# Kernel tuning notes

Hardware: AMD Instinct MI355X
Metric: run time of the kernel (lower is better)

The kernel has to match this reference:

```python
import jax, jax.numpy as jnp
import numpy as np

D_MODEL = 1024
N_HEADS = 16
HEAD_DIM = D_MODEL // N_HEADS


def setup_inputs() -> dict:
    key = jax.random.key(0)
    k_x, k_wqkv, k_bqkv, k_wo, k_bo = jax.random.split(key, 5)
    lim_qkv = 1.0 / np.sqrt(D_MODEL)
    return {
        "x": jax.random.normal(k_x, (2, 4096, D_MODEL), dtype=jnp.float32),
        "w_qkv": jax.random.uniform(k_wqkv, (D_MODEL, 3 * D_MODEL), minval=-lim_qkv, maxval=lim_qkv, dtype=jnp.float32),
        "b_qkv": jax.random.uniform(k_bqkv, (3 * D_MODEL,), minval=-lim_qkv, maxval=lim_qkv, dtype=jnp.float32),
        "w_out": jax.random.uniform(k_wo, (D_MODEL, D_MODEL), minval=-lim_qkv, maxval=lim_qkv, dtype=jnp.float32),
        "b_out": jax.random.uniform(k_bo, (D_MODEL,), minval=-lim_qkv, maxval=lim_qkv, dtype=jnp.float32),
    }


def reference(x, w_qkv, b_qkv, w_out, b_out):
    b, s, _ = x.shape
    scale = HEAD_DIM ** -0.5
    qkv = x @ w_qkv + b_qkv                              # [b, s, 3*d]
    qkv = qkv.reshape(b, s, 3, N_HEADS, HEAD_DIM)
    qkv = jnp.transpose(qkv, (2, 0, 3, 1, 4))            # [3, b, h, s, hd]
    q, k, v = qkv[0], qkv[1], qkv[2]
    scores = jnp.einsum("bhqd,bhkd->bhqk", q, k) * scale  # [b, h, s, s]
    causal = jnp.triu(jnp.ones((s, s), dtype=bool), k=1)
    scores = jnp.where(causal, -jnp.inf, scores)
    probs = jax.nn.softmax(scores, axis=-1)
    out = jnp.einsum("bhqk,bhkd->bhqd", probs, v)         # [b, h, s, hd]
    out = jnp.transpose(out, (0, 2, 1, 3)).reshape(b, s, D_MODEL)
    return out @ w_out + b_out
```

## Files before the change

### kernel.cpp

```cpp
#include <hip/hip_runtime.h>
#include <math.h>

#define S_LEN 4096
#define DM    1024
#define NHEAD 16
#define HDIM  64
#define C3    3072

typedef __attribute__((ext_vector_type(8))) short bf8_t;
typedef __attribute__((ext_vector_type(4))) float f32x4;
typedef __attribute__((ext_vector_type(16))) float f32x16;

__device__ __forceinline__ short f2bf(float f) {
    union { float f; unsigned u; } v; v.f = f;
    unsigned r = v.u + 0x7FFF + ((v.u >> 16) & 1);
    return (short)(r >> 16);
}
__device__ __forceinline__ float fexp2(float x) { return __builtin_amdgcn_exp2f(x); }

__device__ __forceinline__ unsigned cvtpk(float a, float b) {
    unsigned r;
    asm("v_cvt_pk_bf16_f32 %0, %1, %2" : "=v"(r) : "v"(a), "v"(b));
    return r;
}

__device__ __forceinline__ void gload_lds16(const void* g, void* l) {
    __builtin_amdgcn_global_load_lds(
        (const __attribute__((address_space(1))) unsigned int*)g,
        (__attribute__((address_space(3))) unsigned int*)l, 16, 0, 0);
}

__device__ __forceinline__ float vsum16(f32x16 s) {
    float a = (s[0] + s[1]) + (s[2] + s[3]);
    float b = (s[4] + s[5]) + (s[6] + s[7]);
    float c = (s[8] + s[9]) + (s[10] + s[11]);
    float d = (s[12] + s[13]) + (s[14] + s[15]);
    return (a + b) + (c + d);
}

__global__ void cast_f32_bf16(const float* __restrict__ in, short* __restrict__ out, int n8)
{
    int i = blockIdx.x * blockDim.x + threadIdx.x;
    if (i < n8) {
        float4 a = ((const float4*)in)[i * 2];
        float4 b = ((const float4*)in)[i * 2 + 1];
        bf8_t v = {f2bf(a.x), f2bf(a.y), f2bf(a.z), f2bf(a.w),
                   f2bf(b.x), f2bf(b.y), f2bf(b.z), f2bf(b.w)};
        ((bf8_t*)out)[i] = v;
    }
}

__global__ __launch_bounds__(256)
void transpose_cast(const float* __restrict__ in, short* __restrict__ out, int R, int C)
{
    __shared__ float t[32][33];
    const int tx = threadIdx.x & 31;
    const int ty = threadIdx.x >> 5;
    const int r0 = blockIdx.y * 32;
    const int c0 = blockIdx.x * 32;
    #pragma unroll
    for (int i = 0; i < 32; i += 8)
        t[ty + i][tx] = in[(size_t)(r0 + ty + i) * C + c0 + tx];
    __syncthreads();
    #pragma unroll
    for (int i = 0; i < 32; i += 8)
        out[(size_t)(c0 + ty + i) * R + r0 + tx] = f2bf(t[tx][ty + i]);
}

__global__ __launch_bounds__(256)
void transpose_v(const short* __restrict__ qkv, short* __restrict__ vt)
{
    __shared__ short t[64][72];
    const int st = blockIdx.x, bh = blockIdx.y;
    const int b = bh >> 4, h = bh & 15;
    const int tid = threadIdx.x;
    const int r   = tid >> 2;
    const int c16 = (tid & 3) * 16;
    const short* src = qkv + (size_t)b * S_LEN * C3 + 2 * DM + h * HDIM;
    const short* sp  = src + (size_t)(st * 64 + r) * C3 + c16;
    *(bf8_t*)&t[r][c16]     = *(const bf8_t*)sp;
    *(bf8_t*)&t[r][c16 + 8] = *(const bf8_t*)(sp + 8);
    __syncthreads();
    short tmp[16];
    #pragma unroll
    for (int i = 0; i < 16; ++i) tmp[i] = t[c16 + i][r];
    short* dp = vt + (size_t)bh * HDIM * S_LEN + (size_t)r * S_LEN + st * 64 + c16;
    *(bf8_t*)dp       = *(bf8_t*)&tmp[0];
    *(bf8_t*)(dp + 8) = *(bf8_t*)&tmp[8];
}

template<bool BF16OUT>
__global__ __launch_bounds__(256)
void gemm_mfma(const short* __restrict__ A, const short* __restrict__ Bt,
               const float* __restrict__ bias, void* __restrict__ Cout,
               int M, int N)
{
    constexpr int K = 1024;
    __shared__ __align__(16) short As[128 * 64];
    __shared__ __align__(16) short Bs[128 * 64];

    const int nbx = N / 128;
    const int nwg = (M / 128) * nbx;
    int bid = blockIdx.x;
    bid = (bid & 7) * (nwg >> 3) + (bid >> 3);
    const int by = bid / nbx, bx = bid % nbx;
    const int row0 = by * 128, col0 = bx * 128;

    const int tid  = threadIdx.x;
    const int lane = tid & 63;
    const int w    = tid >> 6;
    const int l15  = lane & 15;
    const int l4   = lane >> 4;
    const int wr   = w >> 1, wc = w & 1;

    f32x4 acc[4][4];
    #pragma unroll
    for (int i = 0; i < 4; ++i)
        #pragma unroll
        for (int j = 0; j < 4; ++j) acc[i][j] = (f32x4){0.f, 0.f, 0.f, 0.f};

    size_t goff[4];
    int    loff[4];
    #pragma unroll
    for (int i = 0; i < 4; ++i) {
        const int o   = (w * 4 + i) * 1024 + lane * 16;
        const int row = o >> 7;
        const int col = (o & 127) ^ ((row & 7) << 4);
        goff[i] = (size_t)row * (K * 2) + col;
        loff[i] = o;
    }
    const char* Ab = (const char*)A  + (size_t)row0 * (K * 2);
    const char* Bb = (const char*)Bt + (size_t)col0 * (K * 2);

    for (int k0 = 0; k0 < K; k0 += 64) {
        __syncthreads();
        #pragma unroll
        for (int i = 0; i < 4; ++i) {
            gload_lds16(Ab + goff[i] + k0 * 2, (char*)As + loff[i]);
            gload_lds16(Bb + goff[i] + k0 * 2, (char*)Bs + loff[i]);
        }
        __syncthreads();

        #pragma unroll
        for (int ks = 0; ks < 2; ++ks) {
            bf8_t af[4], bfr[4];
            #pragma unroll
            for (int mi = 0; mi < 4; ++mi) {
                const int row = wr * 64 + mi * 16 + l15;
                const int off = (row * 128 + ks * 64 + l4 * 16) ^ ((row & 7) << 4);
                af[mi] = *(bf8_t*)((char*)As + off);
            }
            #pragma unroll
            for (int ni = 0; ni < 4; ++ni) {
                const int row = wc * 64 + ni * 16 + l15;
                const int off = (row * 128 + ks * 64 + l4 * 16) ^ ((row & 7) << 4);
                bfr[ni] = *(bf8_t*)((char*)Bs + off);
            }
            #pragma unroll
            for (int mi = 0; mi < 4; ++mi)
                #pragma unroll
                for (int ni = 0; ni < 4; ++ni)
                    acc[mi][ni] = __builtin_amdgcn_mfma_f32_16x16x32_bf16(
                        af[mi], bfr[ni], acc[mi][ni], 0, 0, 0);
        }
    }

    float bv[4];
    #pragma unroll
    for (int ni = 0; ni < 4; ++ni)
        bv[ni] = bias[col0 + wc * 64 + ni * 16 + l15];

    #pragma unroll
    for (int mi = 0; mi < 4; ++mi)
        #pragma unroll
        for (int r = 0; r < 4; ++r) {
            const int row = row0 + wr * 64 + mi * 16 + l4 * 4 + r;
            #pragma unroll
            for (int ni = 0; ni < 4; ++ni) {
                const int col = col0 + wc * 64 + ni * 16 + l15;
                const float val = acc[mi][ni][r] + bv[ni];
                if constexpr (BF16OUT)
                    ((short*)Cout)[(size_t)row * N + col] = f2bf(val);
                else
                    ((float*)Cout)[(size_t)row * N + col] = val;
            }
        }
}

__global__ __launch_bounds__(256)
void attn_mfma32(const short* __restrict__ qkv, const short* __restrict__ vt,
                 short* __restrict__ out)
{
    const int lin = blockIdx.x + 16 * blockIdx.y;
    const int xcd = lin & 7;
    const int idx = lin >> 3;
    const int bh  = xcd * 4 + (idx >> 4);
    const int g   = idx & 15;

    const int b   = bh >> 4, h = bh & 15;
    const int tid = threadIdx.x;
    const int lane = tid & 63;
    const int w    = tid >> 6;
    const int l31  = lane & 31;
    const int hi   = lane >> 5;

    __shared__ __align__(16) short lds[2][2][64 * 64];

    const float C   = 0.125f * 1.44269504f;
    const float NEG = -1e30f;

    const short* qkb = qkv + (size_t)b * S_LEN * C3 + h * HDIM;

    const int sr = tid >> 3;
    const int sc = ((tid & 7) * 16) ^ ((sr & 7) << 4);
    const char* srcK = (const char*)(qkb + DM) + (size_t)sr * (C3 * 2) + sc;
    const char* srcV = (const char*)(vt + (size_t)bh * HDIM * S_LEN)
                       + (size_t)sr * (S_LEN * 2) + sc;
    const int ldst = tid * 16;

    #pragma unroll 1
    for (int half = 0; half < 2; ++half) {
        const int qb     = half ? g : (31 - g);
        const int Q0     = qb * 128;
        const int nkt    = qb * 2 + 2;
        const int qmin_w = Q0 + w * 32;
        const int qmax_w = qmin_w + 31;
        const int q_g    = qmin_w + l31;
        const int nkt_w  = (qmax_w >> 6) + 1;

        bf8_t qf[4];
        {
            const short* qp = qkb + (size_t)q_g * C3 + hi * 8;
            qf[0] = *(const bf8_t*)(qp);
            qf[1] = *(const bf8_t*)(qp + 16);
            qf[2] = *(const bf8_t*)(qp + 32);
            qf[3] = *(const bf8_t*)(qp + 48);
        }

        f32x16 o0, o1;
        #pragma unroll
        for (int r = 0; r < 16; ++r) { o0[r] = 0.f; o1[r] = 0.f; }
        float l = 0.f;

        gload_lds16(srcK,                     (char*)lds + ldst);
        gload_lds16(srcK + 32 * (C3 * 2),     (char*)lds + 4096 + ldst);
        gload_lds16(srcV,                     (char*)lds + 8192 + ldst);
        gload_lds16(srcV + 32 * (S_LEN * 2),  (char*)lds + 12288 + ldst);
        __syncthreads();

        for (int kt = 0; kt < nkt; ++kt) {
            const int cur = kt & 1;
            if (kt + 1 < nkt) {
                const char* sK = srcK + (size_t)(kt + 1) * 64 * (C3 * 2);
                const char* sV = srcV + (size_t)(kt + 1) * 64 * 2;
                char* dstb = (char*)lds + (cur ^ 1) * 16384;
                gload_lds16(sK,                    dstb + ldst);
                gload_lds16(sK + 32 * (C3 * 2),    dstb + 4096 + ldst);
                gload_lds16(sV,                    dstb + 8192 + ldst);
                gload_lds16(sV + 32 * (S_LEN * 2), dstb + 12288 + ldst);
            }

            if (kt < nkt_w) {
                const char* Kb = (char*)lds + cur * 16384;
                const char* Vb = Kb + 8192;
                const int kb0 = kt * 64;
                const bool act1 = (kb0 + 32) <= qmax_w;

                f32x16 s0, s1;
                #pragma unroll
                for (int r = 0; r < 16; ++r) { s0[r] = 0.f; s1[r] = NEG; }
                __builtin_amdgcn_s_setprio(1);
                #pragma unroll
                for (int ds = 0; ds < 4; ++ds) {
                    const int R0 = l31;
                    const int off0 = (R0 * 128 + ds * 32 + hi * 16) ^ ((R0 & 7) << 4);
                    bf8_t kf = *(const bf8_t*)(Kb + off0);
                    s0 = __builtin_amdgcn_mfma_f32_32x32x16_bf16(kf, qf[ds], s0, 0, 0, 0);
                }
                if (act1) {
                    #pragma unroll
                    for (int r = 0; r < 16; ++r) s1[r] = 0.f;
                    #pragma unroll
                    for (int ds = 0; ds < 4; ++ds) {
                        const int R1 = 32 + l31;
                        const int off1 = (R1 * 128 + ds * 32 + hi * 16) ^ ((R1 & 7) << 4);
                        bf8_t kf = *(const bf8_t*)(Kb + off1);
                        s1 = __builtin_amdgcn_mfma_f32_32x32x16_bf16(kf, qf[ds], s1, 0, 0, 0);
                    }
                }
                __builtin_amdgcn_s_setprio(0);

                if (kb0 + 31 > qmin_w) {
                    #pragma unroll
                    for (int r = 0; r < 16; ++r) {
                        const int k = kb0 + 4 * hi + ((r & 3) + 8 * (r >> 2));
                        if (k > q_g) s0[r] = NEG;
                    }
                }
                if (act1 && (kb0 + 63 > qmin_w)) {
                    #pragma unroll
                    for (int r = 0; r < 16; ++r) {
                        const int k = kb0 + 32 + 4 * hi + ((r & 3) + 8 * (r >> 2));
                        if (k > q_g) s1[r] = NEG;
                    }
                }

                #pragma unroll
                for (int r = 0; r < 16; ++r) s0[r] = fexp2(s0[r] * C);
                #pragma unroll
                for (int r = 0; r < 16; ++r) s1[r] = fexp2(s1[r] * C);

                l += vsum16(s0) + vsum16(s1);

                unsigned W0[2][4], W1[2][4];
                #pragma unroll
                for (int gg = 0; gg < 4; ++gg) {
                    W0[0][gg] = cvtpk(s0[4 * gg], s0[4 * gg + 1]);
                    W1[0][gg] = cvtpk(s0[4 * gg + 2], s0[4 * gg + 3]);
                    W0[1][gg] = cvtpk(s1[4 * gg], s1[4 * gg + 1]);
                    W1[1][gg] = cvtpk(s1[4 * gg + 2], s1[4 * gg + 3]);
                }

                #pragma unroll
                for (int c = 0; c < 4; ++c) {
                    const int t  = c >> 1;
                    const int gA = 2 * (c & 1);
                    const int gB = gA + 1;
                    const unsigned rx0 = __shfl_xor(hi ? W0[t][gA] : W0[t][gB], 32);
                    const unsigned rx1 = __shfl_xor(hi ? W1[t][gA] : W1[t][gB], 32);
                    union { unsigned u[4]; bf8_t v; } pf;
                    pf.u[0] = hi ? rx0 : W0[t][gA];
                    pf.u[1] = hi ? rx1 : W1[t][gA];
                    pf.u[2] = hi ? W0[t][gB] : rx0;
                    pf.u[3] = hi ? W1[t][gB] : rx1;

                    __builtin_amdgcn_s_setprio(1);
                    {
                        const int R = l31;
                        const int off = (R * 128 + c * 32 + hi * 16) ^ ((R & 7) << 4);
                        bf8_t vf = *(const bf8_t*)(Vb + off);
                        o0 = __builtin_amdgcn_mfma_f32_32x32x16_bf16(pf.v, vf, o0, 0, 0, 0);
                    }
                    {
                        const int R = 32 + l31;
                        const int off = (R * 128 + c * 32 + hi * 16) ^ ((R & 7) << 4);
                        bf8_t vf = *(const bf8_t*)(Vb + off);
                        o1 = __builtin_amdgcn_mfma_f32_32x32x16_bf16(pf.v, vf, o1, 0, 0, 0);
                    }
                    __builtin_amdgcn_s_setprio(0);
                }
            }
            __syncthreads();
        }

        const float lt = l + __shfl_xor(l, 32);
        const float inv = 1.f / lt;
        #pragma unroll
        for (int r = 0; r < 16; ++r) {
            const int cr = 4 * hi + ((r & 3) + 8 * (r >> 2));
            const float iv = __shfl(inv, cr);
            const int row = Q0 + w * 32 + cr;
            short* op = out + (size_t)(b * S_LEN + row) * DM + h * HDIM + l31;
            op[0]  = f2bf(o0[r] * iv);
            op[32] = f2bf(o1[r] * iv);
        }
    }
}

extern "C" void kernel_launch(void* const* d_in, const int* in_sizes, int n_in,
                              void* d_out, int out_size, void* d_ws, size_t ws_size,
                              hipStream_t stream)
{
    const float* x     = (const float*)d_in[0];
    const float* w_qkv = (const float*)d_in[1];
    const float* b_qkv = (const float*)d_in[2];
    const float* w_out = (const float*)d_in[3];
    const float* b_out = (const float*)d_in[4];
    float* out = (float*)d_out;

    const int M = 2 * S_LEN;

    char* ws = (char*)d_ws;
    short* qkvb  = (short*)(ws);
    short* attnb = (short*)(ws + 50331648);
    short* xb    = (short*)(ws + 67108864);
    short* wqkvT = (short*)(ws + 83886080);
    short* woutT = (short*)(ws + 90177536);
    short* vtb   = (short*)(ws + 92274688);

    cast_f32_bf16<<<dim3((M * DM / 8 + 255) / 256), 256, 0, stream>>>(x, xb, M * DM / 8);
    transpose_cast<<<dim3(C3 / 32, DM / 32), 256, 0, stream>>>(w_qkv, wqkvT, DM, C3);
    transpose_cast<<<dim3(DM / 32, DM / 32), 256, 0, stream>>>(w_out, woutT, DM, DM);

    gemm_mfma<true><<<dim3((M / 128) * (C3 / 128)), 256, 0, stream>>>(
        xb, wqkvT, b_qkv, qkvb, M, C3);

    transpose_v<<<dim3(S_LEN / 64, 2 * NHEAD), 256, 0, stream>>>(qkvb, vtb);

    attn_mfma32<<<dim3(16, 2 * NHEAD), 256, 0, stream>>>(qkvb, vtb, attnb);

    gemm_mfma<false><<<dim3((M / 128) * (DM / 128)), 256, 0, stream>>>(
        attnb, woutT, b_out, out, M, DM);
}
```

Baseline: 224.0 us.

## Software-pipeline attention loop: overlap PV of previous tile with QK softmax

Restructures the attention inner loop so the PV MFMAs for tile kt-1 are issued between the QK MFMAs and the softmax/exp work of tile kt. The aim is to let the matrix units run while the vector units compute exp and pack. To keep the previous tile's V resident, LDS goes from double to triple buffering, and the packed probabilities are carried across iterations in registers. A tail step handles the final tile's PV. The change adds register pressure and LDS use, and it carries a correctness risk in the epilogue condition.

```diff
diff --git a/kernel.cpp b/kernel.cpp
--- a/kernel.cpp
+++ b/kernel.cpp
@@ -204,7 +204,7 @@
     const int l31  = lane & 31;
     const int hi   = lane >> 5;
 
-    __shared__ __align__(16) short lds[2][2][64 * 64];
+    __shared__ __align__(16) char lds[3][16384];
 
     const float C   = 0.125f * 1.44269504f;
     const float NEG = -1e30f;
@@ -241,32 +241,35 @@
         #pragma unroll
         for (int r = 0; r < 16; ++r) { o0[r] = 0.f; o1[r] = 0.f; }
         float l = 0.f;
-
-        gload_lds16(srcK,                     (char*)lds + ldst);
-        gload_lds16(srcK + 32 * (C3 * 2),     (char*)lds + 4096 + ldst);
-        gload_lds16(srcV,                     (char*)lds + 8192 + ldst);
-        gload_lds16(srcV + 32 * (S_LEN * 2),  (char*)lds + 12288 + ldst);
+        unsigned Pf[4][4];
+
+        gload_lds16(srcK,                     lds[0] + ldst);
+        gload_lds16(srcK + 32 * (C3 * 2),     lds[0] + 4096 + ldst);
+        gload_lds16(srcV,                     lds[0] + 8192 + ldst);
+        gload_lds16(srcV + 32 * (S_LEN * 2),  lds[0] + 12288 + ldst);
         __syncthreads();
 
+        int cur = 0;
+        #pragma unroll 1
         for (int kt = 0; kt < nkt; ++kt) {
-            const int cur = kt & 1;
+            const int nxt = (cur == 2) ? 0 : cur + 1;
+            const int prv = (cur == 0) ? 2 : cur - 1;
+
             if (kt + 1 < nkt) {
                 const char* sK = srcK + (size_t)(kt + 1) * 64 * (C3 * 2);
                 const char* sV = srcV + (size_t)(kt + 1) * 64 * 2;
-                char* dstb = (char*)lds + (cur ^ 1) * 16384;
-                gload_lds16(sK,                    dstb + ldst);
-                gload_lds16(sK + 32 * (C3 * 2),    dstb + 4096 + ldst);
-                gload_lds16(sV,                    dstb + 8192 + ldst);
-                gload_lds16(sV + 32 * (S_LEN * 2), dstb + 12288 + ldst);
-            }
-
-            if (kt < nkt_w) {
-                const char* Kb = (char*)lds + cur * 16384;
-                const char* Vb = Kb + 8192;
-                const int kb0 = kt * 64;
-                const bool act1 = (kb0 + 32) <= qmax_w;
-
-                f32x16 s0, s1;
+                char* d = lds[nxt];
+                gload_lds16(sK,                    d + ldst);
+                gload_lds16(sK + 32 * (C3 * 2),    d + 4096 + ldst);
+                gload_lds16(sV,                    d + 8192 + ldst);
+                gload_lds16(sV + 32 * (S_LEN * 2), d + 12288 + ldst);
+            }
+
+            const bool doqk = (kt < nkt_w);
+            f32x16 s0, s1;
+
+            if (doqk) {
+                const char* Kb = lds[cur];
                 #pragma unroll
                 for (int r = 0; r < 16; ++r) { s0[r] = 0.f; s1[r] = NEG; }
                 __builtin_amdgcn_s_setprio(1);
@@ -277,7 +280,8 @@
                     bf8_t kf = *(const bf8_t*)(Kb + off0);
                     s0 = __builtin_amdgcn_mfma_f32_32x32x16_bf16(kf, qf[ds], s0, 0, 0, 0);
                 }
-                if (act1) {
+                const int kb0 = kt * 64;
+                if ((kb0 + 32) <= qmax_w) {
                     #pragma unroll
                     for (int r = 0; r < 16; ++r) s1[r] = 0.f;
                     #pragma unroll
@@ -289,52 +293,18 @@
                     }
                 }
                 __builtin_amdgcn_s_setprio(0);
-
-                if (kb0 + 31 > qmin_w) {
-                    #pragma unroll
-                    for (int r = 0; r < 16; ++r) {
-                        const int k = kb0 + 4 * hi + ((r & 3) + 8 * (r >> 2));
-                        if (k > q_g) s0[r] = NEG;
-                    }
-                }
-                if (act1 && (kb0 + 63 > qmin_w)) {
-                    #pragma unroll
-                    for (int r = 0; r < 16; ++r) {
-                        const int k = kb0 + 32 + 4 * hi + ((r & 3) + 8 * (r >> 2));
-                        if (k > q_g) s1[r] = NEG;
-                    }
-                }
-
-                #pragma unroll
-                for (int r = 0; r < 16; ++r) s0[r] = fexp2(s0[r] * C);
-                #pragma unroll
-                for (int r = 0; r < 16; ++r) s1[r] = fexp2(s1[r] * C);
-
-                l += vsum16(s0) + vsum16(s1);
-
-                unsigned W0[2][4], W1[2][4];
-                #pragma unroll
-                for (int gg = 0; gg < 4; ++gg) {
-                    W0[0][gg] = cvtpk(s0[4 * gg], s0[4 * gg + 1]);
-                    W1[0][gg] = cvtpk(s0[4 * gg + 2], s0[4 * gg + 3]);
-                    W0[1][gg] = cvtpk(s1[4 * gg], s1[4 * gg + 1]);
-                    W1[1][gg] = cvtpk(s1[4 * gg + 2], s1[4 * gg + 3]);
-                }
-
+            }
+
+            if (kt >= 1 && kt <= nkt_w) {
+                const char* Vb = lds[prv] + 8192;
+                __builtin_amdgcn_s_setprio(1);
                 #pragma unroll
                 for (int c = 0; c < 4; ++c) {
-                    const int t  = c >> 1;
-                    const int gA = 2 * (c & 1);
-                    const int gB = gA + 1;
-                    const unsigned rx0 = __shfl_xor(hi ? W0[t][gA] : W0[t][gB], 32);
-                    const unsigned rx1 = __shfl_xor(hi ? W1[t][gA] : W1[t][gB], 32);
                     union { unsigned u[4]; bf8_t v; } pf;
-                    pf.u[0] = hi ? rx0 : W0[t][gA];
-                    pf.u[1] = hi ? rx1 : W1[t][gA];
-                    pf.u[2] = hi ? W0[t][gB] : rx0;
-                    pf.u[3] = hi ? W1[t][gB] : rx1;
-
-                    __builtin_amdgcn_s_setprio(1);
+                    pf.u[0] = Pf[c][0];
+                    pf.u[1] = Pf[c][1];
+                    pf.u[2] = Pf[c][2];
+                    pf.u[3] = Pf[c][3];
                     {
                         const int R = l31;
                         const int off = (R * 128 + c * 32 + hi * 16) ^ ((R & 7) << 4);
@@ -347,10 +317,83 @@
                         bf8_t vf = *(const bf8_t*)(Vb + off);
                         o1 = __builtin_amdgcn_mfma_f32_32x32x16_bf16(pf.v, vf, o1, 0, 0, 0);
                     }
-                    __builtin_amdgcn_s_setprio(0);
-                }
-            }
+                }
+                __builtin_amdgcn_s_setprio(0);
+            }
+
+            if (doqk) {
+                const int kb0 = kt * 64;
+                if (kb0 + 31 > qmin_w) {
+                    #pragma unroll
+                    for (int r = 0; r < 16; ++r) {
+                        const int k = kb0 + 4 * hi + ((r & 3) + 8 * (r >> 2));
+                        if (k > q_g) s0[r] = NEG;
+                    }
+                }
+                if (((kb0 + 32) <= qmax_w) && (kb0 + 63 > qmin_w)) {
+                    #pragma unroll
+                    for (int r = 0; r < 16; ++r) {
+                        const int k = kb0 + 32 + 4 * hi + ((r & 3) + 8 * (r >> 2));
+                        if (k > q_g) s1[r] = NEG;
+                    }
+                }
+
+                #pragma unroll
+                for (int r = 0; r < 16; ++r) s0[r] = fexp2(s0[r] * C);
+                #pragma unroll
+                for (int r = 0; r < 16; ++r) s1[r] = fexp2(s1[r] * C);
+
+                l += vsum16(s0) + vsum16(s1);
+
+                unsigned W0[2][4], W1[2][4];
+                #pragma unroll
+                for (int gg = 0; gg < 4; ++gg) {
+                    W0[0][gg] = cvtpk(s0[4 * gg], s0[4 * gg + 1]);
+                    W1[0][gg] = cvtpk(s0[4 * gg + 2], s0[4 * gg + 3]);
+                    W0[1][gg] = cvtpk(s1[4 * gg], s1[4 * gg + 1]);
+                    W1[1][gg] = cvtpk(s1[4 * gg + 2], s1[4 * gg + 3]);
+                }
+                #pragma unroll
+                for (int c = 0; c < 4; ++c) {
+                    const int t  = c >> 1;
+                    const int gA = 2 * (c & 1);
+                    const int gB = gA + 1;
+                    const unsigned rx0 = __shfl_xor(hi ? W0[t][gA] : W0[t][gB], 32);
+                    const unsigned rx1 = __shfl_xor(hi ? W1[t][gA] : W1[t][gB], 32);
+                    Pf[c][0] = hi ? rx0 : W0[t][gA];
+                    Pf[c][1] = hi ? rx1 : W1[t][gA];
+                    Pf[c][2] = hi ? W0[t][gB] : rx0;
+                    Pf[c][3] = hi ? W1[t][gB] : rx1;
+                }
+            }
+
             __syncthreads();
+            cur = nxt;
+        }
+
+        if (nkt_w == nkt) {
+            const int prv = (cur == 0) ? 2 : cur - 1;
+            const char* Vb = lds[prv] + 8192;
+            #pragma unroll
+            for (int c = 0; c < 4; ++c) {
+                union { unsigned u[4]; bf8_t v; } pf;
+                pf.u[0] = Pf[c][0];
+                pf.u[1] = Pf[c][1];
+                pf.u[2] = Pf[c][2];
+                pf.u[3] = Pf[c][3];
+                {
+                    const int R = l31;
+                    const int off = (R * 128 + c * 32 + hi * 16) ^ ((R & 7) << 4);
+                    bf8_t vf = *(const bf8_t*)(Vb + off);
+                    o0 = __builtin_amdgcn_mfma_f32_32x32x16_bf16(pf.v, vf, o0, 0, 0, 0);
+                }
+                {
+                    const int R = 32 + l31;
+                    const int off = (R * 128 + c * 32 + hi * 16) ^ ((R & 7) << 4);
+                    bf8_t vf = *(const bf8_t*)(Vb + off);
+                    o1 = __builtin_amdgcn_mfma_f32_32x32x16_bf16(pf.v, vf, o1, 0, 0, 0);
+                }
+            }
         }
 
         const float lt = l + __shfl_xor(l, 32);
@@ -364,6 +407,8 @@
             op[0]  = f2bf(o0[r] * iv);
             op[32] = f2bf(o1[r] * iv);
         }
+
+        __syncthreads();
     }
 }
 
```

Result: slower. 231.8 us (+3.5%).
